# Kernel tuning notes

Hardware: AMD Instinct MI355X
Metric: run time of the kernel (lower is better)

Reference implementation:

```python
import jax, jax.numpy as jnp
import numpy as np
from jax import lax

B, C_IN, L = 512, 32, 512
E = 8
POOL = 16            # AdaptiveAvgPool1d(16)
D_IN = C_IN * L      # expert input = flattened x
D_OUT = 768          # pooler_output dim (hard-coded in module)
TAU = 1.0            # gumbel temperature
BN_EPS = 1e-5


def setup_inputs() -> dict:
    key = jax.random.key(0)
    ks = jax.random.split(key, 8)
    s = 0.02
    return {
        "x": jax.random.normal(ks[0], (B, C_IN, L), jnp.float32),
        "gumbel_u": jax.random.uniform(ks[1], (B, E), jnp.float32, 1e-6, 1.0 - 1e-6),
        "conv_w": jax.random.normal(ks[2], (64, C_IN, 3), jnp.float32) * s,
        "conv_b": jnp.zeros((64,), jnp.float32),
        "bn_gamma": jnp.ones((64 * POOL,), jnp.float32),
        "bn_beta": jnp.zeros((64 * POOL,), jnp.float32),
        "bn_mean": jnp.zeros((64 * POOL,), jnp.float32),
        "bn_var": jnp.ones((64 * POOL,), jnp.float32),
        "fc1_w": jax.random.normal(ks[3], (128, 64 * POOL), jnp.float32) * s,
        "fc1_b": jnp.zeros((128,), jnp.float32),
        "fc2_w": jax.random.normal(ks[4], (E, 128), jnp.float32) * s,
        "fc2_b": jnp.zeros((E,), jnp.float32),
        "expert_w": jax.random.normal(ks[5], (E, D_IN, D_OUT), jnp.float32) * s,
        "expert_b": jnp.zeros((E, D_OUT), jnp.float32),
    }


def _gelu(v):
    return jax.nn.gelu(v, approximate=False)  # torch nn.GELU default (erf)


def reference(x, gumbel_u, conv_w, conv_b, bn_gamma, bn_beta, bn_mean, bn_var,
              fc1_w, fc1_b, fc2_w, fc2_b, expert_w, expert_b):
    # ---- router ----
    h = lax.conv_general_dilated(x, conv_w, (1,), ((1, 1),),
                                 dimension_numbers=("NCH", "OIH", "NCH"))
    h = _gelu(h + conv_b[None, :, None])                     # [B,64,L]
    h = h.reshape(B, 64, POOL, L // POOL).mean(-1)           # adaptive avg pool -> [B,64,16]
    h = h.reshape(B, 64 * POOL)                              # flatten
    h = (h - bn_mean) * lax.rsqrt(bn_var + BN_EPS) * bn_gamma + bn_beta  # BN (eval)
    h = _gelu(h @ fc1_w.T + fc1_b)                           # dropout inactive in eval
    logits = h @ fc2_w.T + fc2_b                             # [B,E]

    # ---- soft gumbel-softmax gating (hard=False), then top-2 ----
    g = -jnp.log(-jnp.log(gumbel_u))
    routing_weights = jax.nn.softmax((logits + g) / TAU, axis=1)
    topv, topi = lax.top_k(routing_weights, 2)               # [B,2]
    w = topv / (topv.sum(axis=1, keepdims=True) + 1e-8)      # [B,2]

    # ---- dispatch/compute/combine (dense-expert stand-in: flatten + linear) ----
    xf = x.reshape(B, D_IN)
    all_out = jnp.einsum("bd,edh->beh", xf, expert_w) + expert_b[None]  # [B,E,768]
    sel = jnp.take_along_axis(all_out, topi[:, :, None], axis=1)        # [B,2,768]
    pooler_output = (sel * w[:, :, None]).sum(axis=1)                   # [B,768]
    return pooler_output
```

## Files before the change

### kernel.cpp

```cpp
#include <hip/hip_runtime.h>
#include <hip/hip_bf16.h>

#define NB 512
#define CIN 32
#define LEN 512
#define NE 8
#define NPOOL 16
#define DIN 16384
#define DOUT 768
#define HD 1024
#define F1 128

#define MT 256
#define NT 64
#define BK 32

typedef __attribute__((ext_vector_type(4))) float f32x4;
typedef __attribute__((ext_vector_type(8))) short s16x8;
typedef __attribute__((ext_vector_type(4))) unsigned int u32x4;

__device__ __forceinline__ float gelu_erf(float v) {
    return 0.5f * v * (1.0f + erff(v * 0.70710678118654752f));
}

__device__ __forceinline__ unsigned cvt_pk(float lo, float hi) {
    unsigned r;
    asm volatile("v_cvt_pk_bf16_f32 %0, %1, %2" : "=v"(r) : "v"(lo), "v"(hi));
    return r;
}

__device__ __forceinline__ unsigned short f2bf_u(float f) {
    union { float f; unsigned u; } x; x.f = f;
    unsigned r = x.u + 0x7fffu + ((x.u >> 16) & 1u);
    return (unsigned short)(r >> 16);
}

__device__ __forceinline__ void gload_lds16(const void* gptr, void* lptr) {
    __builtin_amdgcn_global_load_lds(
        (const __attribute__((address_space(1))) unsigned int*)gptr,
        (__attribute__((address_space(3))) unsigned int*)lptr,
        16, 0, 0);
}

__global__ __launch_bounds__(256) void kcvt(const float* __restrict__ x,
                                            unsigned short* __restrict__ xb)
{
    int i = blockIdx.x * 256 + threadIdx.x;
    const f32x4* src = (const f32x4*)(x + (size_t)i * 8);
    f32x4 v0 = src[0], v1 = src[1];
    u32x4 pk;
    pk[0] = cvt_pk(v0[0], v0[1]); pk[1] = cvt_pk(v0[2], v0[3]);
    pk[2] = cvt_pk(v1[0], v1[1]); pk[3] = cvt_pk(v1[2], v1[3]);
    *(u32x4*)(xb + (size_t)i * 8) = pk;
}

__global__ __launch_bounds__(256) void krouter_conv(
    const float* __restrict__ x, const float* __restrict__ cw, const float* __restrict__ cb,
    const float* __restrict__ bng, const float* __restrict__ bnb,
    const float* __restrict__ bnm, const float* __restrict__ bnv,
    float* __restrict__ h, int* __restrict__ cnt)
{
    __shared__ float xs[CIN * 264];
    int half = blockIdx.x;
    int b = blockIdx.y;
    int t = threadIdx.x;
    if (b == 0 && half == 0 && t < NE) cnt[t] = 0;

    int Lchunk0 = half * 64 - 1;
    const float* xb_ = x + (size_t)b * DIN;
    for (int idx = t; idx < CIN * 66; idx += 256) {
        int ci = idx / 66;
        int cc = idx - ci * 66;
        int gc = min(max(Lchunk0 + cc, 0), 127);
        f32x4 v = *(const f32x4*)(xb_ + ci * 512 + gc * 4);
        int byte = ci * 1056 + ((cc << 4) ^ (((cc >> 3) & 7) << 4));
        *(f32x4*)((char*)xs + byte) = v;
    }
    __syncthreads();

    int p  = t & 7;
    int pg = half * 8 + p;
    int cq = t >> 3;
    int co0 = cq * 2, co1 = co0 + 1;

    float sa[32], sb[32];
    #pragma unroll
    for (int i = 0; i < 32; ++i) { sa[i] = 0.f; sb[i] = 0.f; }

    for (int ci = 0; ci < CIN; ++ci) {
        float f[40];
        #pragma unroll
        for (int u = 0; u < 10; ++u) {
            int lc = p * 8 + u;
            int byte = ci * 1056 + ((lc << 4) ^ (((lc >> 3) & 7) << 4));
            f32x4 v = *(const f32x4*)((const char*)xs + byte);
            f[4*u+0] = v[0]; f[4*u+1] = v[1]; f[4*u+2] = v[2]; f[4*u+3] = v[3];
        }
        if (pg == 0)  f[3]  = 0.f;
        if (pg == 15) f[36] = 0.f;
        float wa0 = cw[co0*96 + ci*3 + 0], wa1 = cw[co0*96 + ci*3 + 1], wa2 = cw[co0*96 + ci*3 + 2];
        float wb0 = cw[co1*96 + ci*3 + 0], wb1 = cw[co1*96 + ci*3 + 1], wb2 = cw[co1*96 + ci*3 + 2];
        #pragma unroll
        for (int i = 0; i < 32; ++i) {
            sa[i] = fmaf(f[i+3], wa0, fmaf(f[i+4], wa1, fmaf(f[i+5], wa2, sa[i])));
            sb[i] = fmaf(f[i+3], wb0, fmaf(f[i+4], wb1, fmaf(f[i+5], wb2, sb[i])));
        }
    }

    float ba = cb[co0], bbv = cb[co1];
    float ma = 0.f, mb = 0.f;
    #pragma unroll
    for (int i = 0; i < 32; ++i) { ma += gelu_erf(sa[i] + ba); mb += gelu_erf(sb[i] + bbv); }
    ma *= (1.f / 32.f); mb *= (1.f / 32.f);

    int oa = co0 * NPOOL + pg, ob = co1 * NPOOL + pg;
    float ra = (ma - bnm[oa]) * rsqrtf(bnv[oa] + 1e-5f) * bng[oa] + bnb[oa];
    float rb = (mb - bnm[ob]) * rsqrtf(bnv[ob] + 1e-5f) * bng[ob] + bnb[ob];
    h[(size_t)b * HD + oa] = ra;
    h[(size_t)b * HD + ob] = rb;
}

__global__ __launch_bounds__(256) void krouter_fc(
    const float* __restrict__ h, const float* __restrict__ f1w, const float* __restrict__ f1b,
    const float* __restrict__ f2w, const float* __restrict__ f2b,
    const float* __restrict__ gu,
    int* __restrict__ top2e, float* __restrict__ top2w,
    int* __restrict__ cnt, int* __restrict__ rowlist, float* __restrict__ roww)
{
    __shared__ float hs[8 * HD];
    __shared__ float h1s[8 * F1];
    __shared__ float lg[8 * NE];

    int bb = blockIdx.x * 8;
    int t = threadIdx.x;

    const f32x4* hg = (const f32x4*)(h + (size_t)bb * HD);
    f32x4* hs4 = (f32x4*)hs;
    #pragma unroll
    for (int u = 0; u < 8; ++u) hs4[t + 256 * u] = hg[t + 256 * u];
    __syncthreads();

    int j = t & 127;
    int pr = t >> 7;
    float acc[4] = {0.f, 0.f, 0.f, 0.f};
    const f32x4* w4 = (const f32x4*)(f1w + (size_t)j * HD);
    for (int k4 = 0; k4 < 256; ++k4) {
        f32x4 w = w4[k4];
        #pragma unroll
        for (int g = 0; g < 4; ++g) {
            f32x4 hv = hs4[(pr * 4 + g) * 256 + k4];
            acc[g] += w[0]*hv[0] + w[1]*hv[1] + w[2]*hv[2] + w[3]*hv[3];
        }
    }
    float bj = f1b[j];
    #pragma unroll
    for (int g = 0; g < 4; ++g) h1s[(pr * 4 + g) * F1 + j] = gelu_erf(acc[g] + bj);
    __syncthreads();

    if (t < 64) {
        int bi = t >> 3, e = t & 7;
        float s = f2b[e];
        const float* w = f2w + e * F1;
        const float* hh = h1s + bi * F1;
        #pragma unroll 8
        for (int k = 0; k < F1; ++k) s += hh[k] * w[k];
        lg[bi * NE + e] = s;
    }
    __syncthreads();

    if (t < 8) {
        int bi = t; int b = bb + bi;
        float r[NE];
        float mx = -1e30f;
        #pragma unroll
        for (int e = 0; e < NE; ++e) {
            float g = -logf(-logf(gu[b * NE + e]));
            r[e] = lg[bi * NE + e] + g;
            mx = fmaxf(mx, r[e]);
        }
        float sum = 0.f;
        #pragma unroll
        for (int e = 0; e < NE; ++e) { r[e] = expf(r[e] - mx); sum += r[e]; }
        float inv = 1.f / sum;
        #pragma unroll
        for (int e = 0; e < NE; ++e) r[e] *= inv;
        int e0 = 0; float v0 = r[0];
        #pragma unroll
        for (int e = 1; e < NE; ++e) if (r[e] > v0) { v0 = r[e]; e0 = e; }
        int e1 = -1; float v1 = -1.f;
        #pragma unroll
        for (int e = 0; e < NE; ++e) { if (e == e0) continue; if (r[e] > v1) { v1 = r[e]; e1 = e; } }
        float den = v0 + v1 + 1e-8f;
        float w0 = v0 / den, w1 = v1 / den;
        top2e[b * 2 + 0] = e0; top2e[b * 2 + 1] = e1;
        top2w[b * 2 + 0] = w0; top2w[b * 2 + 1] = w1;
        int p0 = atomicAdd(&cnt[e0], 1);
        rowlist[e0 * NB + p0] = b * 2 + 0; roww[e0 * NB + p0] = w0;
        int p1 = atomicAdd(&cnt[e1], 1);
        rowlist[e1 * NB + p1] = b * 2 + 1; roww[e1 * NB + p1] = w1;
    }
}

__global__ __launch_bounds__(512, 2) void kgemm(
    const unsigned short* __restrict__ xb, const float* __restrict__ ew,
    const int* __restrict__ cnt, const int* __restrict__ rowlist, const float* __restrict__ roww,
    unsigned short* __restrict__ ypart, int nkc, int kch)
{
    int nwg = gridDim.x;
    int cpx = nwg >> 3;
    int wg = (blockIdx.x & 7) * cpx + (blockIdx.x >> 3);
    int nt = wg % 12;
    int kc = (wg / 12) % nkc;
    int e  = wg / (12 * nkc);
    int cn = cnt[e];

    __shared__ __align__(16) char As[2][MT * BK * 2];
    __shared__ __align__(16) char Bs[2][BK * NT * 4];

    int t = threadIdx.x;
    int wid = t >> 6, lane = t & 63;
    int wm = wid >> 1, wn = wid & 1;
    int g = lane >> 4;
    int NS = kch / BK;
    int k0 = kc * kch;

    const char* gB = (const char*)ew + (size_t)e * DIN * DOUT * 4
                   + (size_t)k0 * (DOUT * 4) + nt * NT * 4;
    int bk_ = wid * 4 + (lane >> 4);
    int bc_ = lane & 15;
    int bkey = ((bk_ >> 3) & 3) << 2;
    const char* gp = gB + (size_t)bk_ * (DOUT * 4) + ((bc_ ^ bkey) << 4);
    int ldsB = wid * 1024;

    int ar = t >> 1, ah = t & 1;
    int akey_ = (ar >> 1) & 3;
    int ach0 = ((2 * ah) ^ akey_) << 4;
    int ach1 = ((2 * ah + 1) ^ akey_) << 4;

    for (int row0 = 0; row0 < cn; row0 += MT) {
        int mloc = min(MT, cn - row0);
        int arc = min(ar, mloc - 1);
        int ent_a = rowlist[e * NB + row0 + arc];
        const char* axp = (const char*)xb
                        + ((size_t)(ent_a >> 1) * DIN + k0) * 2 + ah * 32;
        bool ado = (ar < mloc);
        bool wact = (wm * 64 < mloc);

        f32x4 acc[4][2];
        #pragma unroll
        for (int i = 0; i < 4; ++i)
            #pragma unroll
            for (int jj = 0; jj < 2; ++jj) acc[i][jj] = (f32x4){0.f, 0.f, 0.f, 0.f};

        u32x4 A0, A1;
        const char* bp = gp;

        auto loadA = [&](int s) {
            if (ado) {
                const u32x4* p = (const u32x4*)(axp + (size_t)s * (BK * 2));
                A0 = p[0]; A1 = p[1];
            }
        };
        auto stageB = [&](int bi) {
            gload_lds16(bp, (char*)Bs[bi] + ldsB);
        };
        auto storeA = [&](int bi) {
            if (ado) {
                *(u32x4*)(As[bi] + ar * 64 + ach0) = A0;
                *(u32x4*)(As[bi] + ar * 64 + ach1) = A1;
            }
        };

        loadA(0);
        stageB(0);
        storeA(0);
        __syncthreads();

        for (int s = 0; s < NS; ++s) {
            int buf = s & 1;
            if (s + 1 < NS) {
                loadA(s + 1);
                bp += (size_t)BK * DOUT * 4;
                stageB(buf ^ 1);
            }

            if (wact) {
                const char* Ab = As[buf];
                const char* Bb = Bs[buf];
                s16x8 af[4];
                #pragma unroll
                for (int mi = 0; mi < 4; ++mi) {
                    int m = wm * 64 + mi * 16 + (lane & 15);
                    af[mi] = *(const s16x8*)(Ab + m * 64 + ((g ^ ((m >> 1) & 3)) << 4));
                }
                #pragma unroll
                for (int ni = 0; ni < 2; ++ni) {
                    int n = wn * 32 + ni * 16 + (lane & 15);
                    int cb = (((n >> 2) ^ (g << 2)) << 4) + ((n & 3) << 2);
                    float v[8];
                    #pragma unroll
                    for (int j = 0; j < 8; ++j)
                        v[j] = *(const float*)(Bb + (g * 8 + j) * 256 + cb);
                    union { u32x4 u; s16x8 s; } bf;
                    bf.u[0] = cvt_pk(v[0], v[1]); bf.u[1] = cvt_pk(v[2], v[3]);
                    bf.u[2] = cvt_pk(v[4], v[5]); bf.u[3] = cvt_pk(v[6], v[7]);
                    #pragma unroll
                    for (int mi = 0; mi < 4; ++mi)
                        acc[mi][ni] = __builtin_amdgcn_mfma_f32_16x16x32_bf16(af[mi], bf.s, acc[mi][ni], 0, 0, 0);
                }
            }

            __builtin_amdgcn_sched_barrier(0);
            if (s + 1 < NS) storeA(buf ^ 1);
            __syncthreads();
        }

        if (wact) {
            #pragma unroll
            for (int mi = 0; mi < 4; ++mi) {
                #pragma unroll
                for (int rg = 0; rg < 4; ++rg) {
                    int m = wm * 64 + mi * 16 + g * 4 + rg;
                    if (m < mloc) {
                        int ent = rowlist[e * NB + row0 + m];
                        float wgt = roww[e * NB + row0 + m];
                        int ob = ent >> 1, slot = ent & 1;
                        unsigned short* dst = ypart + ((size_t)(slot * nkc + kc) * NB + ob) * DOUT
                                            + nt * NT + wn * 32 + (lane & 15);
                        #pragma unroll
                        for (int ni = 0; ni < 2; ++ni)
                            dst[ni * 16] = f2bf_u(acc[mi][ni][rg] * wgt);
                    }
                }
            }
        }
        __syncthreads();
    }
}

__global__ __launch_bounds__(256) void kcombine(
    const unsigned short* __restrict__ ypart,
    const int* __restrict__ top2e, const float* __restrict__ top2w,
    const float* __restrict__ eb, float* __restrict__ out, int nplanes)
{
    int b = blockIdx.y;
    int n = blockIdx.x * 256 + threadIdx.x;
    float s = 0.f;
    for (int p = 0; p < nplanes; ++p) {
        unsigned v = ypart[((size_t)p * NB + b) * DOUT + n];
        union { unsigned u; float f; } c; c.u = v << 16;
        s += c.f;
    }
    int e0 = top2e[b * 2], e1 = top2e[b * 2 + 1];
    float w0 = top2w[b * 2], w1 = top2w[b * 2 + 1];
    s += w0 * eb[e0 * DOUT + n] + w1 * eb[e1 * DOUT + n];
    out[(size_t)b * DOUT + n] = s;
}

extern "C" void kernel_launch(void* const* d_in, const int* in_sizes, int n_in,
                              void* d_out, int out_size, void* d_ws, size_t ws_size,
                              hipStream_t stream)
{
    const float* x   = (const float*)d_in[0];
    const float* gu  = (const float*)d_in[1];
    const float* cw  = (const float*)d_in[2];
    const float* cb  = (const float*)d_in[3];
    const float* bng = (const float*)d_in[4];
    const float* bnb = (const float*)d_in[5];
    const float* bnm = (const float*)d_in[6];
    const float* bnv = (const float*)d_in[7];
    const float* f1w = (const float*)d_in[8];
    const float* f1b = (const float*)d_in[9];
    const float* f2w = (const float*)d_in[10];
    const float* f2b = (const float*)d_in[11];
    const float* ew  = (const float*)d_in[12];
    const float* eb  = (const float*)d_in[13];

    int nkc = (ws_size >= (size_t)64 * 1024 * 1024) ? 16 : 8;
    int kch = DIN / nkc;

    char* ws = (char*)d_ws;
    size_t off = 0;
    float* h       = (float*)(ws + off); off += (size_t)NB * HD * 4;
    int*   top2e   = (int*)(ws + off);   off += (size_t)NB * 2 * 4;
    float* top2w   = (float*)(ws + off); off += (size_t)NB * 2 * 4;
    int*   cnt     = (int*)(ws + off);   off += 256;
    int*   rowlist = (int*)(ws + off);   off += (size_t)NE * NB * 4;
    float* roww    = (float*)(ws + off); off += (size_t)NE * NB * 4;
    unsigned short* xbuf = (unsigned short*)(ws + off);
    off += (size_t)NB * DIN * 2;
    unsigned short* ypart = (unsigned short*)(ws + off);
    off += (size_t)2 * nkc * NB * DOUT * 2;

    kcvt<<<(NB * DIN / 8 + 255) / 256, 256, 0, stream>>>(x, xbuf);
    krouter_conv<<<dim3(2, NB), 256, 0, stream>>>(x, cw, cb, bng, bnb, bnm, bnv, h, cnt);
    krouter_fc<<<NB / 8, 256, 0, stream>>>(h, f1w, f1b, f2w, f2b, gu,
                                           top2e, top2w, cnt, rowlist, roww);
    kgemm<<<NE * nkc * 12, 512, 0, stream>>>(xbuf, ew, cnt, rowlist, roww, ypart, nkc, kch);
    kcombine<<<dim3(3, NB), 256, 0, stream>>>(ypart, top2e, top2w, eb, (float*)d_out, 2 * nkc);
}
```

Measured before the change: 263.2 us.

## Fuse x bf16 conversion into grouped GEMM and deepen B-tile pipeline

Drops the separate fp32-to-bf16 conversion kernel for x. The GEMM now loads fp32 activation rows straight from global memory into registers (gathered through the row list) and converts them in-register, so the A tile no longer goes through shared memory. B staging moves to a 4-deep LDS ring with explicit vmcnt waits and one barrier per step. The M tile shrinks to 192 and occupancy is raised to 4 blocks per CU. The trade is double the bytes read for A per k-step and more register pressure from the direct fp32 loads, in exchange for removing a full pass over x and the LDS traffic for A.

New measurement: 351.7 us. 1.34x slower.

```diff
diff --git a/kernel.cpp b/kernel.cpp
--- a/kernel.cpp
+++ b/kernel.cpp
@@ -11,9 +11,10 @@
 #define HD 1024
 #define F1 128
 
-#define MT 256
+#define MT 192
 #define NT 64
 #define BK 32
+#define NBUF 4
 
 typedef __attribute__((ext_vector_type(4))) float f32x4;
 typedef __attribute__((ext_vector_type(8))) short s16x8;
@@ -40,18 +41,6 @@
         (const __attribute__((address_space(1))) unsigned int*)gptr,
         (__attribute__((address_space(3))) unsigned int*)lptr,
         16, 0, 0);
-}
-
-__global__ __launch_bounds__(256) void kcvt(const float* __restrict__ x,
-                                            unsigned short* __restrict__ xb)
-{
-    int i = blockIdx.x * 256 + threadIdx.x;
-    const f32x4* src = (const f32x4*)(x + (size_t)i * 8);
-    f32x4 v0 = src[0], v1 = src[1];
-    u32x4 pk;
-    pk[0] = cvt_pk(v0[0], v0[1]); pk[1] = cvt_pk(v0[2], v0[3]);
-    pk[2] = cvt_pk(v1[0], v1[1]); pk[3] = cvt_pk(v1[2], v1[3]);
-    *(u32x4*)(xb + (size_t)i * 8) = pk;
 }
 
 __global__ __launch_bounds__(256) void krouter_conv(
@@ -201,8 +190,8 @@
     }
 }
 
-__global__ __launch_bounds__(512, 2) void kgemm(
-    const unsigned short* __restrict__ xb, const float* __restrict__ ew,
+__global__ __launch_bounds__(512, 4) void kgemm(
+    const float* __restrict__ x, const float* __restrict__ ew,
     const int* __restrict__ cnt, const int* __restrict__ rowlist, const float* __restrict__ roww,
     unsigned short* __restrict__ ypart, int nkc, int kch)
 {
@@ -214,8 +203,7 @@
     int e  = wg / (12 * nkc);
     int cn = cnt[e];
 
-    __shared__ __align__(16) char As[2][MT * BK * 2];
-    __shared__ __align__(16) char Bs[2][BK * NT * 4];
+    __shared__ __align__(16) char Bs[NBUF][BK * NT * 4];
 
     int t = threadIdx.x;
     int wid = t >> 6, lane = t & 63;
@@ -232,67 +220,68 @@
     const char* gp = gB + (size_t)bk_ * (DOUT * 4) + ((bc_ ^ bkey) << 4);
     int ldsB = wid * 1024;
 
-    int ar = t >> 1, ah = t & 1;
-    int akey_ = (ar >> 1) & 3;
-    int ach0 = ((2 * ah) ^ akey_) << 4;
-    int ach1 = ((2 * ah + 1) ^ akey_) << 4;
+    const float* xk = x + k0 + g * 8;
 
     for (int row0 = 0; row0 < cn; row0 += MT) {
         int mloc = min(MT, cn - row0);
-        int arc = min(ar, mloc - 1);
-        int ent_a = rowlist[e * NB + row0 + arc];
-        const char* axp = (const char*)xb
-                        + ((size_t)(ent_a >> 1) * DIN + k0) * 2 + ah * 32;
-        bool ado = (ar < mloc);
-        bool wact = (wm * 64 < mloc);
-
-        f32x4 acc[4][2];
-        #pragma unroll
-        for (int i = 0; i < 4; ++i)
+        bool wact = (wm * 48 < mloc);
+
+        size_t abase[3];
+        #pragma unroll
+        for (int mi = 0; mi < 3; ++mi) {
+            int m = wm * 48 + mi * 16 + (lane & 15);
+            int mc = min(m, mloc - 1);
+            abase[mi] = (size_t)(rowlist[e * NB + row0 + mc] >> 1) * DIN;
+        }
+
+        f32x4 acc[3][2];
+        #pragma unroll
+        for (int i = 0; i < 3; ++i)
             #pragma unroll
             for (int jj = 0; jj < 2; ++jj) acc[i][jj] = (f32x4){0.f, 0.f, 0.f, 0.f};
 
-        u32x4 A0, A1;
+        f32x4 An[3][2];
         const char* bp = gp;
 
         auto loadA = [&](int s) {
-            if (ado) {
-                const u32x4* p = (const u32x4*)(axp + (size_t)s * (BK * 2));
-                A0 = p[0]; A1 = p[1];
+            #pragma unroll
+            for (int mi = 0; mi < 3; ++mi) {
+                const f32x4* p = (const f32x4*)(xk + abase[mi] + s * BK);
+                An[mi][0] = p[0]; An[mi][1] = p[1];
             }
         };
-        auto stageB = [&](int bi) {
-            gload_lds16(bp, (char*)Bs[bi] + ldsB);
+        auto stageB = [&](int s) {
+            gload_lds16(bp + (size_t)s * (BK * DOUT * 4), (char*)Bs[s & (NBUF - 1)] + ldsB);
         };
-        auto storeA = [&](int bi) {
-            if (ado) {
-                *(u32x4*)(As[bi] + ar * 64 + ach0) = A0;
-                *(u32x4*)(As[bi] + ar * 64 + ach1) = A1;
+
+        stageB(0);
+        loadA(0);
+        if (1 < NS) stageB(1);
+
+        for (int s = 0; s < NS; ++s) {
+            s16x8 af[3];
+            #pragma unroll
+            for (int mi = 0; mi < 3; ++mi) {
+                union { u32x4 u; s16x8 v; } c;
+                c.u[0] = cvt_pk(An[mi][0][0], An[mi][0][1]);
+                c.u[1] = cvt_pk(An[mi][0][2], An[mi][0][3]);
+                c.u[2] = cvt_pk(An[mi][1][0], An[mi][1][1]);
+                c.u[3] = cvt_pk(An[mi][1][2], An[mi][1][3]);
+                af[mi] = c.v;
             }
-        };
-
-        loadA(0);
-        stageB(0);
-        storeA(0);
-        __syncthreads();
-
-        for (int s = 0; s < NS; ++s) {
-            int buf = s & 1;
-            if (s + 1 < NS) {
-                loadA(s + 1);
-                bp += (size_t)BK * DOUT * 4;
-                stageB(buf ^ 1);
-            }
+            if (s + 1 < NS) loadA(s + 1);
+            if (s + 2 < NS) stageB(s + 2);
+            __builtin_amdgcn_sched_barrier(0);
+            if (s + 2 < NS)      asm volatile("s_waitcnt vmcnt(8)" ::: "memory");
+            else if (s + 1 < NS) asm volatile("s_waitcnt vmcnt(7)" ::: "memory");
+            else                 asm volatile("s_waitcnt vmcnt(0)" ::: "memory");
+            __builtin_amdgcn_sched_barrier(0);
+            __builtin_amdgcn_s_barrier();
+            __builtin_amdgcn_sched_barrier(0);
 
             if (wact) {
-                const char* Ab = As[buf];
-                const char* Bb = Bs[buf];
-                s16x8 af[4];
-                #pragma unroll
-                for (int mi = 0; mi < 4; ++mi) {
-                    int m = wm * 64 + mi * 16 + (lane & 15);
-                    af[mi] = *(const s16x8*)(Ab + m * 64 + ((g ^ ((m >> 1) & 3)) << 4));
-                }
+                const char* Bb = Bs[s & (NBUF - 1)];
+                __builtin_amdgcn_s_setprio(1);
                 #pragma unroll
                 for (int ni = 0; ni < 2; ++ni) {
                     int n = wn * 32 + ni * 16 + (lane & 15);
@@ -301,26 +290,23 @@
                     #pragma unroll
                     for (int j = 0; j < 8; ++j)
                         v[j] = *(const float*)(Bb + (g * 8 + j) * 256 + cb);
-                    union { u32x4 u; s16x8 s; } bf;
+                    union { u32x4 u; s16x8 v8; } bf;
                     bf.u[0] = cvt_pk(v[0], v[1]); bf.u[1] = cvt_pk(v[2], v[3]);
                     bf.u[2] = cvt_pk(v[4], v[5]); bf.u[3] = cvt_pk(v[6], v[7]);
                     #pragma unroll
-                    for (int mi = 0; mi < 4; ++mi)
-                        acc[mi][ni] = __builtin_amdgcn_mfma_f32_16x16x32_bf16(af[mi], bf.s, acc[mi][ni], 0, 0, 0);
+                    for (int mi = 0; mi < 3; ++mi)
+                        acc[mi][ni] = __builtin_amdgcn_mfma_f32_16x16x32_bf16(af[mi], bf.v8, acc[mi][ni], 0, 0, 0);
                 }
+                __builtin_amdgcn_s_setprio(0);
             }
-
-            __builtin_amdgcn_sched_barrier(0);
-            if (s + 1 < NS) storeA(buf ^ 1);
-            __syncthreads();
         }
 
         if (wact) {
             #pragma unroll
-            for (int mi = 0; mi < 4; ++mi) {
+            for (int mi = 0; mi < 3; ++mi) {
                 #pragma unroll
                 for (int rg = 0; rg < 4; ++rg) {
-                    int m = wm * 64 + mi * 16 + g * 4 + rg;
+                    int m = wm * 48 + mi * 16 + g * 4 + rg;
                     if (m < mloc) {
                         int ent = rowlist[e * NB + row0 + m];
                         float wgt = roww[e * NB + row0 + m];
@@ -376,7 +362,7 @@
     const float* ew  = (const float*)d_in[12];
     const float* eb  = (const float*)d_in[13];
 
-    int nkc = (ws_size >= (size_t)64 * 1024 * 1024) ? 16 : 8;
+    int nkc = (ws_size >= (size_t)40 * 1024 * 1024) ? 16 : 8;
     int kch = DIN / nkc;
 
     char* ws = (char*)d_ws;
@@ -387,15 +373,12 @@
     int*   cnt     = (int*)(ws + off);   off += 256;
     int*   rowlist = (int*)(ws + off);   off += (size_t)NE * NB * 4;
     float* roww    = (float*)(ws + off); off += (size_t)NE * NB * 4;
-    unsigned short* xbuf = (unsigned short*)(ws + off);
-    off += (size_t)NB * DIN * 2;
     unsigned short* ypart = (unsigned short*)(ws + off);
     off += (size_t)2 * nkc * NB * DOUT * 2;
 
-    kcvt<<<(NB * DIN / 8 + 255) / 256, 256, 0, stream>>>(x, xbuf);
     krouter_conv<<<dim3(2, NB), 256, 0, stream>>>(x, cw, cb, bng, bnb, bnm, bnv, h, cnt);
     krouter_fc<<<NB / 8, 256, 0, stream>>>(h, f1w, f1b, f2w, f2b, gu,
                                            top2e, top2w, cnt, rowlist, roww);
-    kgemm<<<NE * nkc * 12, 512, 0, stream>>>(xbuf, ew, cnt, rowlist, roww, ypart, nkc, kch);
+    kgemm<<<NE * nkc * 12, 512, 0, stream>>>(x, ew, cnt, rowlist, roww, ypart, nkc, kch);
     kcombine<<<dim3(3, NB), 256, 0, stream>>>(ypart, top2e, top2w, eb, (float*)d_out, 2 * nkc);
 }
```
